# Kernel tuning notes

Hardware: AMD Instinct MI355X
Metric: run time of the kernel (lower is better)

Reference implementation:

```python
import jax, jax.numpy as jnp
import numpy as np

C_IN = 3072
C_OUT = 1024
MAJ = 3  # majority_size


def setup_inputs() -> dict:
    key = jax.random.key(0)
    k1, k2 = jax.random.split(key)
    x = jax.random.normal(k1, (256, C_IN), dtype=jnp.float32)
    stdv = 1.0 / np.sqrt(C_OUT * C_IN)
    weight = jax.random.uniform(k2, (C_OUT, C_IN), dtype=jnp.float32, minval=-stdv, maxval=stdv)
    return {"input": x, "weight": weight}


def reference(input, weight):
    B = input.shape[0]
    G = C_IN // MAJ  # number of majority groups
    # Deterministic binarization (sign), as in Binarize(..., 'det')
    xb = jnp.sign(input)            # [B, C_IN]
    wb = jnp.sign(weight)           # [C_OUT, C_IN]
    # Grouped products: inter[b,c,g] = sum_k xb[b,g,k] * wb[c,g,k]
    # (equivalent to einsum('bj,cj->bcj') followed by reshape+sum over groups of 3)
    xg = xb.reshape(B, G, MAJ)
    wg = wb.reshape(C_OUT, G, MAJ)
    inter = jnp.einsum('bgk,cgk->bcg', xg, wg)  # [B, C_OUT, G]
    # Majority vote: clamp group sums to [-1, 1], sum across groups, scale by 2.25
    out = jnp.sum(jnp.clip(inter, -1.0, 1.0), axis=2) * 2.25  # [B, C_OUT]
    return out
```

## Files before the change

kernel.cpp:

```cpp
#include <hip/hip_runtime.h>
#include <stdint.h>


#define C_IN  3072
#define C_OUT 1024
#define CHUNKS_W 4096
#define CHUNKS_TOT 5120


__global__ __launch_bounds__(256) void pack_signs(const float* __restrict__ x,
                                                  const float* __restrict__ w,
                                                  uint64_t* __restrict__ wpk,
                                                  uint64_t* __restrict__ xpk) {
    int j    = blockIdx.x * 4 + (threadIdx.x >> 6);
    int lane = threadIdx.x & 63;
    const float* src;
    uint64_t* dst;
    if (j < CHUNKS_W) {
        int c = j >> 2, q = j & 3;
        src = w + (size_t)c * C_IN + q * 768;
        dst = wpk + ((size_t)q * C_OUT + c) * 12;
    } else {
        int id = j - CHUNKS_W;
        int b = id >> 2, q = id & 3;
        src = x + (size_t)b * C_IN + q * 768;
        dst = xpk + ((size_t)b * 4 + q) * 12;
    }
    const float4* s4 = (const float4*)(src + 12 * lane);
    float4 f0 = s4[0], f1 = s4[1], f2 = s4[2];
    float v[12] = {f0.x, f0.y, f0.z, f0.w,
                   f1.x, f1.y, f1.z, f1.w,
                   f2.x, f2.y, f2.z, f2.w};
    uint64_t pl[12];
#pragma unroll
    for (int m = 0; m < 12; ++m)
        pl[m] = __ballot(v[m] > 0.0f);
    if (lane == 0) {
#pragma unroll
        for (int m = 0; m < 12; ++m)
            dst[m] = pl[m];
    }
}

__global__ __launch_bounds__(256) void maj_main(const uint64_t* __restrict__ wpk,
                                                const uint64_t* __restrict__ xpk,
                                                float* __restrict__ out) {
    int tid = threadIdx.x;
    int blk = blockIdx.x;
    int b0  = (blk >> 2) * 2;
    int c   = (blk & 3) * 256 + tid;

    int acc0 = 0, acc1 = 0;
#pragma unroll
    for (int q = 0; q < 4; ++q) {
        const uint64_t* wb = wpk + ((size_t)q * C_OUT + c) * 12;
        const uint64_t* x0 = xpk + ((size_t)(b0 + 0) * 4 + q) * 12;
        const uint64_t* x1 = xpk + ((size_t)(b0 + 1) * 4 + q) * 12;
        uint64_t Wv[12];
#pragma unroll
        for (int m = 0; m < 12; ++m) Wv[m] = wb[m];
#pragma unroll
        for (int j = 0; j < 4; ++j) {
            uint64_t t0 = x0[3 * j + 0] ^ Wv[3 * j + 0];
            uint64_t t1 = x0[3 * j + 1] ^ Wv[3 * j + 1];
            uint64_t t2 = x0[3 * j + 2] ^ Wv[3 * j + 2];
            acc0 += __popcll((t0 & t1) | (t2 & (t0 | t1)));
            uint64_t u0 = x1[3 * j + 0] ^ Wv[3 * j + 0];
            uint64_t u1 = x1[3 * j + 1] ^ Wv[3 * j + 1];
            uint64_t u2 = x1[3 * j + 2] ^ Wv[3 * j + 2];
            acc1 += __popcll((u0 & u1) | (u2 & (u0 | u1)));
        }
    }
    out[(size_t)(b0 + 0) * C_OUT + c] = 2304.0f - 4.5f * (float)acc0;
    out[(size_t)(b0 + 1) * C_OUT + c] = 2304.0f - 4.5f * (float)acc1;
}

extern "C" void kernel_launch(void* const* d_in, const int* in_sizes, int n_in,
                              void* d_out, int out_size, void* d_ws, size_t ws_size,
                              hipStream_t stream) {
    const float* x = (const float*)d_in[0];
    const float* w = (const float*)d_in[1];
    float* out = (float*)d_out;

    uint64_t* wpk = (uint64_t*)d_ws;
    uint64_t* xpk = (uint64_t*)((char*)d_ws + 393216);

    pack_signs<<<1280, 256, 0, stream>>>(x, w, wpk, xpk);
    maj_main<<<512, 256, 0, stream>>>(wpk, xpk, out);
}
```

Before: 70.33 us.

## Fuse weight sign packing into majority kernel, keep packed bits in LDS

```diff
diff --git a/kernel.cpp b/kernel.cpp
--- a/kernel.cpp
+++ b/kernel.cpp
@@ -4,29 +4,14 @@
 
 #define C_IN  3072
 #define C_OUT 1024
-#define CHUNKS_W 4096
-#define CHUNKS_TOT 5120
 
 
-__global__ __launch_bounds__(256) void pack_signs(const float* __restrict__ x,
-                                                  const float* __restrict__ w,
-                                                  uint64_t* __restrict__ wpk,
-                                                  uint64_t* __restrict__ xpk) {
+__global__ __launch_bounds__(256) void pack_x(const float* __restrict__ x,
+                                              uint64_t* __restrict__ xpk) {
     int j    = blockIdx.x * 4 + (threadIdx.x >> 6);
     int lane = threadIdx.x & 63;
-    const float* src;
-    uint64_t* dst;
-    if (j < CHUNKS_W) {
-        int c = j >> 2, q = j & 3;
-        src = w + (size_t)c * C_IN + q * 768;
-        dst = wpk + ((size_t)q * C_OUT + c) * 12;
-    } else {
-        int id = j - CHUNKS_W;
-        int b = id >> 2, q = id & 3;
-        src = x + (size_t)b * C_IN + q * 768;
-        dst = xpk + ((size_t)b * 4 + q) * 12;
-    }
-    const float4* s4 = (const float4*)(src + 12 * lane);
+    int b = j >> 2, q = j & 3;
+    const float4* s4 = (const float4*)(x + (size_t)b * C_IN + q * 768 + 12 * lane);
     float4 f0 = s4[0], f1 = s4[1], f2 = s4[2];
     float v[12] = {f0.x, f0.y, f0.z, f0.w,
                    f1.x, f1.y, f1.z, f1.w,
@@ -36,43 +21,65 @@
     for (int m = 0; m < 12; ++m)
         pl[m] = __ballot(v[m] > 0.0f);
     if (lane == 0) {
+        uint64_t* dst = xpk + ((size_t)b * 4 + q) * 12;
 #pragma unroll
         for (int m = 0; m < 12; ++m)
             dst[m] = pl[m];
     }
 }
 
-__global__ __launch_bounds__(256) void maj_main(const uint64_t* __restrict__ wpk,
-                                                const uint64_t* __restrict__ xpk,
-                                                float* __restrict__ out) {
-    int tid = threadIdx.x;
-    int blk = blockIdx.x;
-    int b0  = (blk >> 2) * 2;
-    int c   = (blk & 3) * 256 + tid;
+__global__ __launch_bounds__(256) void fused_maj(const float* __restrict__ w,
+                                                 const uint64_t* __restrict__ xpk,
+                                                 float* __restrict__ out) {
+    __shared__ uint64_t wpl[8][12];
+    const int tid  = threadIdx.x;
+    const int lane = tid & 63;
+    const int wv   = tid >> 6;
+    const int c0   = blockIdx.x * 2;
 
+    for (int h = wv; h < 8; h += 4) {
+        int cl = h >> 2, q = h & 3;
+        const float4* s4 = (const float4*)(w + (size_t)(c0 + cl) * C_IN + q * 768 + 12 * lane);
+        float4 f0 = s4[0], f1 = s4[1], f2 = s4[2];
+        float v[12] = {f0.x, f0.y, f0.z, f0.w,
+                       f1.x, f1.y, f1.z, f1.w,
+                       f2.x, f2.y, f2.z, f2.w};
+        uint64_t pl[12];
+#pragma unroll
+        for (int m = 0; m < 12; ++m)
+            pl[m] = __ballot(v[m] > 0.0f);
+        if (lane == 0) {
+#pragma unroll
+            for (int m = 0; m < 12; ++m)
+                wpl[h][m] = pl[m];
+        }
+    }
+    __syncthreads();
+
+    const int b = tid;
     int acc0 = 0, acc1 = 0;
 #pragma unroll
     for (int q = 0; q < 4; ++q) {
-        const uint64_t* wb = wpk + ((size_t)q * C_OUT + c) * 12;
-        const uint64_t* x0 = xpk + ((size_t)(b0 + 0) * 4 + q) * 12;
-        const uint64_t* x1 = xpk + ((size_t)(b0 + 1) * 4 + q) * 12;
-        uint64_t Wv[12];
+        const uint64_t* xb = xpk + ((size_t)b * 4 + q) * 12;
+        uint64_t X[12];
 #pragma unroll
-        for (int m = 0; m < 12; ++m) Wv[m] = wb[m];
+        for (int m = 0; m < 12; ++m) X[m] = xb[m];
 #pragma unroll
         for (int j = 0; j < 4; ++j) {
-            uint64_t t0 = x0[3 * j + 0] ^ Wv[3 * j + 0];
-            uint64_t t1 = x0[3 * j + 1] ^ Wv[3 * j + 1];
-            uint64_t t2 = x0[3 * j + 2] ^ Wv[3 * j + 2];
+            uint64_t t0 = X[3 * j + 0] ^ wpl[q][3 * j + 0];
+            uint64_t t1 = X[3 * j + 1] ^ wpl[q][3 * j + 1];
+            uint64_t t2 = X[3 * j + 2] ^ wpl[q][3 * j + 2];
             acc0 += __popcll((t0 & t1) | (t2 & (t0 | t1)));
-            uint64_t u0 = x1[3 * j + 0] ^ Wv[3 * j + 0];
-            uint64_t u1 = x1[3 * j + 1] ^ Wv[3 * j + 1];
-            uint64_t u2 = x1[3 * j + 2] ^ Wv[3 * j + 2];
+            uint64_t u0 = X[3 * j + 0] ^ wpl[4 + q][3 * j + 0];
+            uint64_t u1 = X[3 * j + 1] ^ wpl[4 + q][3 * j + 1];
+            uint64_t u2 = X[3 * j + 2] ^ wpl[4 + q][3 * j + 2];
             acc1 += __popcll((u0 & u1) | (u2 & (u0 | u1)));
         }
     }
-    out[(size_t)(b0 + 0) * C_OUT + c] = 2304.0f - 4.5f * (float)acc0;
-    out[(size_t)(b0 + 1) * C_OUT + c] = 2304.0f - 4.5f * (float)acc1;
+    float2 r;
+    r.x = 2304.0f - 4.5f * (float)acc0;
+    r.y = 2304.0f - 4.5f * (float)acc1;
+    *(float2*)(out + (size_t)b * C_OUT + c0) = r;
 }
 
 extern "C" void kernel_launch(void* const* d_in, const int* in_sizes, int n_in,
@@ -82,9 +89,8 @@
     const float* w = (const float*)d_in[1];
     float* out = (float*)d_out;
 
-    uint64_t* wpk = (uint64_t*)d_ws;
-    uint64_t* xpk = (uint64_t*)((char*)d_ws + 393216);
+    uint64_t* xpk = (uint64_t*)d_ws;
 
-    pack_signs<<<1280, 256, 0, stream>>>(x, w, wpk, xpk);
-    maj_main<<<512, 256, 0, stream>>>(wpk, xpk, out);
+    pack_x<<<256, 256, 0, stream>>>(x, xpk);
+    fused_maj<<<512, 256, 0, stream>>>(w, xpk, out);
 }
```

Result: slower. 73.10 us (+3.9%).
